# Performance work log

Hardware: AMD Instinct MI355X
Metric: run time of the kernel (lower is better)

## Reference

```python
import jax, jax.numpy as jnp
import numpy as np
from jax import lax

BN_EPS = 1e-5


def setup_inputs() -> dict:
    key = jax.random.key(0)
    ks = jax.random.split(key, 3)
    B, N, D = 96, 20, 2048
    return {
        "x": jax.random.normal(ks[0], (B, N, D), dtype=jnp.float32),
        "conv_w": jax.random.normal(ks[1], (D, 2 * D), dtype=jnp.float32) * 0.02,
        "conv_b": jax.random.normal(ks[2], (D,), dtype=jnp.float32) * 0.02,
        "bn_gamma": jnp.ones((D,), dtype=jnp.float32),
        "bn_beta": jnp.zeros((D,), dtype=jnp.float32),
        "bn_mean": jnp.zeros((D,), dtype=jnp.float32),
        "bn_var": jnp.ones((D,), dtype=jnp.float32),
        "n_neighbor": 10,
    }


def reference(x, conv_w, conv_b, bn_gamma, bn_beta, bn_mean, bn_var, n_neighbor):
    # x: [B, N, D] -> xt: [B, D, N] (channels-first point cloud of view features)
    xt = jnp.transpose(x, (0, 2, 1))
    B, D, N = xt.shape
    k = int(n_neighbor)

    # pairwise squared distances: [B, N, N]
    sq = jnp.sum(xt * xt, axis=1, keepdims=True)            # [B, 1, N]
    inner = jnp.einsum("bdn,bdm->bnm", xt, xt)              # [B, N, N]
    adj = sq + (-2.0) * inner + jnp.transpose(sq, (0, 2, 1))

    # k nearest neighbors (smallest distance) -> idx [B, N, k]
    _, nn_idx = lax.top_k(-adj, k)

    # gather neighbor features without the O(N^2) expand: [B, D, N, k]
    neighbors = jax.vmap(lambda xb, idx: xb[:, idx])(xt, nn_idx)

    center = xt[:, :, :, None]                              # [B, D, N, 1]
    edge = jnp.concatenate(
        [jnp.broadcast_to(center, (B, D, N, k)), neighbors - center], axis=1
    )                                                       # [B, 2D, N, k]

    # 1x1 conv (GEMM over channel dim) + BatchNorm (inference) + ReLU
    y = jnp.einsum("oc,bcnk->bonk", conv_w, edge) + conv_b[None, :, None, None]
    inv = bn_gamma / jnp.sqrt(bn_var + BN_EPS)
    y = y * inv[None, :, None, None] + (bn_beta - bn_mean * inv)[None, :, None, None]
    y = jax.nn.relu(y)

    # max over neighbors, then max over points -> [B, D, 1, 1]
    y = jnp.max(y, axis=-1, keepdims=True)
    y = jnp.max(y, axis=2, keepdims=True)
    return y
```

## Files before the change

### kernel.cpp

```cpp
#include <hip/hip_runtime.h>
#include <hip/hip_bf16.h>
#include <math.h>

#define BN_EPS 1e-5f
#define B_  96
#define N_  20
#define D_  2048
#define K_  10
#define M_  (B_*N_)
#define R_  (2*D_)

typedef __attribute__((ext_vector_type(8))) short bf16x8;
typedef __attribute__((ext_vector_type(4))) float f32x4;
typedef __attribute__((ext_vector_type(8))) unsigned short ushort8;

static __device__ __forceinline__ unsigned short f2bf(float f) {
  unsigned int u = __builtin_bit_cast(unsigned int, f);
  u = u + 0x7fffu + ((u >> 16) & 1u);
  return (unsigned short)(u >> 16);
}

#define GLOAD_LDS16(g, l) \
  __builtin_amdgcn_global_load_lds((const __attribute__((address_space(1))) void*)(g), \
                                   (__attribute__((address_space(3))) void*)(l), 16, 0, 0)

__global__ __launch_bounds__(512, 2) void prep_kernel(const float* __restrict__ x,
                                                      const float* __restrict__ cw,
                                                      int* __restrict__ nn_idx,
                                                      unsigned short* __restrict__ Xb,
                                                      unsigned short* __restrict__ Wn)
{
  int t = threadIdx.x;
  if (blockIdx.x >= B_) {
    int cb = blockIdx.x - B_;
    for (int i = cb*512 + t; i < R_*D_/8; i += 416*512) {
      int r = i >> 8;
      int k = (i & 255) * 8;
      const float* src = cw + (size_t)(r >> 1) * R_ + ((r & 1) << 11) + k;
      float4 a = *(const float4*)src, c = *(const float4*)(src + 4);
      ushort8 o = { f2bf(a.x), f2bf(a.y), f2bf(a.z), f2bf(a.w),
                    f2bf(c.x), f2bf(c.y), f2bf(c.z), f2bf(c.w) };
      *((ushort8*)Wn + i) = o;
    }
    return;
  }
  int b = blockIdx.x, w = t >> 6, lane = t & 63;
  __shared__ float innr[N_*N_];
  __shared__ float adjl[N_*N_];
  const float* xb = x + (size_t)b * N_ * D_;
  int n1 = w, n2 = w + 8, n3 = (w < 4) ? 16 + w : -1;
  float4 c1[8], c2[8], c3[8];
  const float4* p1 = (const float4*)(xb + n1 * D_);
  const float4* p2 = (const float4*)(xb + n2 * D_);
  #pragma unroll
  for (int j = 0; j < 8; ++j) { c1[j] = p1[lane + 64*j]; c2[j] = p2[lane + 64*j]; }
  if (n3 >= 0) {
    const float4* p3 = (const float4*)(xb + n3 * D_);
    #pragma unroll
    for (int j = 0; j < 8; ++j) c3[j] = p3[lane + 64*j];
  }
  for (int m = n1; m < N_; ++m) {
    bool d2 = (m >= n2), d3 = (n3 >= 0) && (m >= n3);
    const float4* pm = (const float4*)(xb + m * D_);
    float s1 = 0.f, s2 = 0.f, s3 = 0.f;
    #pragma unroll
    for (int j = 0; j < 8; ++j) {
      float4 v = pm[lane + 64*j];
      s1 = fmaf(c1[j].x, v.x, fmaf(c1[j].y, v.y, fmaf(c1[j].z, v.z, fmaf(c1[j].w, v.w, s1))));
      if (d2) s2 = fmaf(c2[j].x, v.x, fmaf(c2[j].y, v.y, fmaf(c2[j].z, v.z, fmaf(c2[j].w, v.w, s2))));
      if (d3) s3 = fmaf(c3[j].x, v.x, fmaf(c3[j].y, v.y, fmaf(c3[j].z, v.z, fmaf(c3[j].w, v.w, s3))));
    }
    #pragma unroll
    for (int off = 32; off > 0; off >>= 1) {
      s1 += __shfl_xor(s1, off, 64);
      if (d2) s2 += __shfl_xor(s2, off, 64);
      if (d3) s3 += __shfl_xor(s3, off, 64);
    }
    if (lane == 0) {
      innr[n1*N_+m] = s1; innr[m*N_+n1] = s1;
      if (d2) { innr[n2*N_+m] = s2; innr[m*N_+n2] = s2; }
      if (d3) { innr[n3*N_+m] = s3; innr[m*N_+n3] = s3; }
    }
  }
  __syncthreads();
  for (int p = t; p < N_*N_; p += 512) {
    int n = p / N_, m = p % N_;
    adjl[p] = innr[n*N_+n] + innr[m*N_+m] - 2.f * innr[p];
  }
  __syncthreads();
  if (t < N_) {
    int n = t;
    unsigned mask = 0;
    for (int it = 0; it < K_; ++it) {
      float bv = INFINITY; int bi = 0;
      for (int m = 0; m < N_; ++m) {
        if (!((mask >> m) & 1u)) {
          float v = adjl[n*N_+m];
          if (v < bv) { bv = v; bi = m; }
        }
      }
      mask |= 1u << bi;
      nn_idx[(b*N_ + n)*K_ + it] = bi;
    }
  }
  unsigned short* xo = Xb + (size_t)b * N_ * D_;
  for (int i = t; i < N_*D_/8; i += 512) {
    const float4* src = (const float4*)xb + (size_t)i * 2;
    float4 a = src[0], c = src[1];
    ushort8 o = { f2bf(a.x), f2bf(a.y), f2bf(a.z), f2bf(a.w),
                  f2bf(c.x), f2bf(c.y), f2bf(c.z), f2bf(c.w) };
    *((ushort8*)xo + i) = o;
  }
}

__global__ __launch_bounds__(256, 3) void fused_gemm(
    const unsigned short* __restrict__ Xb, const unsigned short* __restrict__ Wn,
    const int* __restrict__ nn_idx, const float* __restrict__ conv_b,
    const float* __restrict__ gamma, const float* __restrict__ beta,
    const float* __restrict__ mean, const float* __restrict__ var,
    float* __restrict__ out)
{
  __shared__ __align__(16) char smem[53248];
  float* Cl  = (float*)smem;
  int*   idxl = (int*)(smem + 40960);

  int flat = blockIdx.y * 24 + blockIdx.x;
  int nf = (flat & 7) * 96 + (flat >> 3);
  int bx = nf % 24, by = nf / 24;

  int t = threadIdx.x, lane = t & 63, w = t >> 6;
  int m0 = bx * 80, b0 = bx * 4;
  int r0 = by * 128, o0 = by * 64;
  int rowsel = lane & 15, ksel = lane >> 4;

  f32x4 acc[5][2] = {};

  auto stage = [&](int sel, int k0) {
    unsigned short* Asb = (unsigned short*)(smem + sel*26624);
    unsigned short* Bsb = (unsigned short*)(smem + sel*26624 + 10240);
    #pragma unroll
    for (int i = 0; i < 3; ++i) {
      int fl = i*256 + t;
      if (fl < 640) {
        int row = fl >> 3, kc = fl & 7;
        GLOAD_LDS16(Xb + (size_t)(m0 + row) * D_ + k0 + ((kc ^ (row & 7)) << 3),
                    Asb + fl*8);
      }
    }
    #pragma unroll
    for (int i = 0; i < 4; ++i) {
      int fl = i*256 + t;
      int row = fl >> 3, kc = fl & 7;
      GLOAD_LDS16(Wn + (size_t)(r0 + row) * D_ + k0 + ((kc ^ (row & 7)) << 3),
                  Bsb + fl*8);
    }
  };

  auto compute = [&](int sel) {
    unsigned short* Asb = (unsigned short*)(smem + sel*26624);
    unsigned short* Bsb = (unsigned short*)(smem + sel*26624 + 10240);
    #pragma unroll
    for (int ks = 0; ks < 2; ++ks) {
      int swz = ((ks*4 + ksel) ^ (rowsel & 7)) << 3;
      bf16x8 a[5], bfr[2];
      #pragma unroll
      for (int mi = 0; mi < 5; ++mi)
        a[mi] = *(const bf16x8*)(Asb + (mi*16 + rowsel)*64 + swz);
      #pragma unroll
      for (int ri = 0; ri < 2; ++ri)
        bfr[ri] = *(const bf16x8*)(Bsb + (w*32 + ri*16 + rowsel)*64 + swz);
      #pragma unroll
      for (int mi = 0; mi < 5; ++mi)
        #pragma unroll
        for (int ri = 0; ri < 2; ++ri)
          acc[mi][ri] = __builtin_amdgcn_mfma_f32_16x16x32_bf16(a[mi], bfr[ri], acc[mi][ri], 0, 0, 0);
    }
  };

  stage(0, 0);
  #pragma unroll 1
  for (int kt = 0; kt < D_/64; ++kt) {
    __builtin_amdgcn_s_barrier();
    __builtin_amdgcn_sched_barrier(0);
    if (kt + 1 < D_/64) {
      stage((kt+1) & 1, (kt+1)*64);
      if (w < 2) { asm volatile("s_waitcnt vmcnt(7)" ::: "memory"); }
      else       { asm volatile("s_waitcnt vmcnt(6)" ::: "memory"); }
    } else {
      asm volatile("s_waitcnt vmcnt(0)" ::: "memory");
    }
    __builtin_amdgcn_sched_barrier(0);
    __builtin_amdgcn_s_barrier();
    __builtin_amdgcn_sched_barrier(0);
    compute(kt & 1);
  }
  __syncthreads();

  #pragma unroll
  for (int mi = 0; mi < 5; ++mi)
    #pragma unroll
    for (int ri = 0; ri < 2; ++ri)
      #pragma unroll
      for (int rg = 0; rg < 4; ++rg)
        Cl[(mi*16 + ksel*4 + rg)*128 + w*32 + ri*16 + rowsel] = acc[mi][ri][rg];
  for (int i = t; i < 4*N_*K_; i += 256) idxl[i] = nn_idx[b0*N_*K_ + i];
  __syncthreads();

  int bb = w, oo = lane;
  int og = o0 + oo;
  float invv  = gamma[og] / sqrtf(var[og] + BN_EPS);
  float shift = fmaf(-mean[og], invv, beta[og]);
  float bias  = conv_b[og];
  float best = 0.f;
  int rbase = bb * N_;
  for (int n = 0; n < N_; ++n) {
    float Pv = Cl[(rbase + n)*128 + oo*2];
    float Qn = Cl[(rbase + n)*128 + oo*2 + 1];
    float aa = Pv - Qn + bias;
    const int* ix = idxl + bb*N_*K_ + n*K_;
    #pragma unroll
    for (int kk = 0; kk < K_; ++kk) {
      int j = ix[kk];
      float v = fmaf(aa + Cl[(rbase + j)*128 + oo*2 + 1], invv, shift);
      best = fmaxf(best, v);
    }
  }
  out[(size_t)(b0 + bb) * D_ + og] = best;
}

extern "C" void kernel_launch(void* const* d_in, const int* in_sizes, int n_in,
                              void* d_out, int out_size, void* d_ws, size_t ws_size,
                              hipStream_t stream)
{
  const float* x      = (const float*)d_in[0];
  const float* conv_w = (const float*)d_in[1];
  const float* conv_b = (const float*)d_in[2];
  const float* gamma  = (const float*)d_in[3];
  const float* beta   = (const float*)d_in[4];
  const float* mean   = (const float*)d_in[5];
  const float* var    = (const float*)d_in[6];

  int* nn_idx = (int*)d_ws;
  unsigned short* Xb = (unsigned short*)((char*)d_ws + 76800);
  unsigned short* Wn = (unsigned short*)((char*)d_ws + 76800 + (size_t)M_*D_*2);

  prep_kernel<<<512, 512, 0, stream>>>(x, conv_w, nn_idx, Xb, Wn);
  fused_gemm<<<dim3(24, 32), 256, 0, stream>>>(
      Xb, Wn, nn_idx, conv_b, gamma, beta, mean, var, (float*)d_out);
}
```

Measured before the change: 78.59 us.

## Load GEMM weight fragments directly into registers and widen weight conversion grid

```diff
diff --git a/kernel.cpp b/kernel.cpp
--- a/kernel.cpp
+++ b/kernel.cpp
@@ -32,16 +32,31 @@
 {
   int t = threadIdx.x;
   if (blockIdx.x >= B_) {
-    int cb = blockIdx.x - B_;
-    for (int i = cb*512 + t; i < R_*D_/8; i += 416*512) {
-      int r = i >> 8;
-      int k = (i & 255) * 8;
-      const float* src = cw + (size_t)(r >> 1) * R_ + ((r & 1) << 11) + k;
-      float4 a = *(const float4*)src, c = *(const float4*)(src + 4);
-      ushort8 o = { f2bf(a.x), f2bf(a.y), f2bf(a.z), f2bf(a.w),
-                    f2bf(c.x), f2bf(c.y), f2bf(c.z), f2bf(c.w) };
-      *((ushort8*)Wn + i) = o;
-    }
+    int i0 = (blockIdx.x - B_) * 512 + t;
+    auto srcp = [&](int i) {
+      int r = i >> 8, k = (i & 255) * 8;
+      return cw + (size_t)(r >> 1) * R_ + ((r & 1) << 11) + k;
+    };
+    const float* s0 = srcp(i0);
+    const float* s1 = srcp(i0 + 262144);
+    const float* s2 = srcp(i0 + 524288);
+    const float* s3 = srcp(i0 + 786432);
+    float4 a0 = *(const float4*)s0, c0 = *(const float4*)(s0 + 4);
+    float4 a1 = *(const float4*)s1, c1 = *(const float4*)(s1 + 4);
+    float4 a2 = *(const float4*)s2, c2 = *(const float4*)(s2 + 4);
+    float4 a3 = *(const float4*)s3, c3 = *(const float4*)(s3 + 4);
+    ushort8 o0 = { f2bf(a0.x), f2bf(a0.y), f2bf(a0.z), f2bf(a0.w),
+                   f2bf(c0.x), f2bf(c0.y), f2bf(c0.z), f2bf(c0.w) };
+    ushort8 o1 = { f2bf(a1.x), f2bf(a1.y), f2bf(a1.z), f2bf(a1.w),
+                   f2bf(c1.x), f2bf(c1.y), f2bf(c1.z), f2bf(c1.w) };
+    ushort8 o2 = { f2bf(a2.x), f2bf(a2.y), f2bf(a2.z), f2bf(a2.w),
+                   f2bf(c2.x), f2bf(c2.y), f2bf(c2.z), f2bf(c2.w) };
+    ushort8 o3 = { f2bf(a3.x), f2bf(a3.y), f2bf(a3.z), f2bf(a3.w),
+                   f2bf(c3.x), f2bf(c3.y), f2bf(c3.z), f2bf(c3.w) };
+    *((ushort8*)Wn + i0)          = o0;
+    *((ushort8*)Wn + i0 + 262144) = o1;
+    *((ushort8*)Wn + i0 + 524288) = o2;
+    *((ushort8*)Wn + i0 + 786432) = o3;
     return;
   }
   int b = blockIdx.x, w = t >> 6, lane = t & 63;
@@ -120,7 +135,7 @@
     const float* __restrict__ mean, const float* __restrict__ var,
     float* __restrict__ out)
 {
-  __shared__ __align__(16) char smem[53248];
+  __shared__ __align__(16) char smem[44160];
   float* Cl  = (float*)smem;
   int*   idxl = (int*)(smem + 40960);
 
@@ -135,9 +150,10 @@
 
   f32x4 acc[5][2] = {};
 
-  auto stage = [&](int sel, int k0) {
-    unsigned short* Asb = (unsigned short*)(smem + sel*26624);
-    unsigned short* Bsb = (unsigned short*)(smem + sel*26624 + 10240);
+  const unsigned short* wnBase = Wn + (size_t)(r0 + w*32 + rowsel) * D_ + ksel*8;
+
+  auto stageA = [&](int sel, int k0) {
+    unsigned short* Asb = (unsigned short*)(smem + sel*10240);
     #pragma unroll
     for (int i = 0; i < 3; ++i) {
       int fl = i*256 + t;
@@ -147,54 +163,46 @@
                     Asb + fl*8);
       }
     }
-    #pragma unroll
-    for (int i = 0; i < 4; ++i) {
-      int fl = i*256 + t;
-      int row = fl >> 3, kc = fl & 7;
-      GLOAD_LDS16(Wn + (size_t)(r0 + row) * D_ + k0 + ((kc ^ (row & 7)) << 3),
-                  Bsb + fl*8);
-    }
   };
 
-  auto compute = [&](int sel) {
-    unsigned short* Asb = (unsigned short*)(smem + sel*26624);
-    unsigned short* Bsb = (unsigned short*)(smem + sel*26624 + 10240);
+  auto loadB = [&](bf16x8 (&bb)[2][2], int kt) {
+    #pragma unroll
+    for (int ri = 0; ri < 2; ++ri)
+      #pragma unroll
+      for (int ks = 0; ks < 2; ++ks)
+        bb[ri][ks] = *(const bf16x8*)(wnBase + (size_t)(ri*16) * D_ + kt*64 + ks*32);
+  };
+
+  auto computeStep = [&](int sel, const bf16x8 (&bb)[2][2]) {
+    unsigned short* Asb = (unsigned short*)(smem + sel*10240);
     #pragma unroll
     for (int ks = 0; ks < 2; ++ks) {
       int swz = ((ks*4 + ksel) ^ (rowsel & 7)) << 3;
-      bf16x8 a[5], bfr[2];
+      bf16x8 a[5];
       #pragma unroll
       for (int mi = 0; mi < 5; ++mi)
         a[mi] = *(const bf16x8*)(Asb + (mi*16 + rowsel)*64 + swz);
-      #pragma unroll
-      for (int ri = 0; ri < 2; ++ri)
-        bfr[ri] = *(const bf16x8*)(Bsb + (w*32 + ri*16 + rowsel)*64 + swz);
       #pragma unroll
       for (int mi = 0; mi < 5; ++mi)
         #pragma unroll
         for (int ri = 0; ri < 2; ++ri)
-          acc[mi][ri] = __builtin_amdgcn_mfma_f32_16x16x32_bf16(a[mi], bfr[ri], acc[mi][ri], 0, 0, 0);
+          acc[mi][ri] = __builtin_amdgcn_mfma_f32_16x16x32_bf16(a[mi], bb[ri][ks], acc[mi][ri], 0, 0, 0);
     }
   };
 
-  stage(0, 0);
+  bf16x8 bEven[2][2], bOdd[2][2];
+  stageA(0, 0);
+  loadB(bEven, 0);
+  __syncthreads();
   #pragma unroll 1
-  for (int kt = 0; kt < D_/64; ++kt) {
-    __builtin_amdgcn_s_barrier();
-    __builtin_amdgcn_sched_barrier(0);
-    if (kt + 1 < D_/64) {
-      stage((kt+1) & 1, (kt+1)*64);
-      if (w < 2) { asm volatile("s_waitcnt vmcnt(7)" ::: "memory"); }
-      else       { asm volatile("s_waitcnt vmcnt(6)" ::: "memory"); }
-    } else {
-      asm volatile("s_waitcnt vmcnt(0)" ::: "memory");
-    }
-    __builtin_amdgcn_sched_barrier(0);
-    __builtin_amdgcn_s_barrier();
-    __builtin_amdgcn_sched_barrier(0);
-    compute(kt & 1);
-  }
-  __syncthreads();
+  for (int kt = 0; kt < D_/64; kt += 2) {
+    if (kt + 1 < D_/64) { stageA(1, (kt+1)*64); loadB(bOdd, kt+1); }
+    computeStep(0, bEven);
+    __syncthreads();
+    if (kt + 2 < D_/64) { stageA(0, (kt+2)*64); loadB(bEven, kt+2); }
+    computeStep(1, bOdd);
+    __syncthreads();
+  }
 
   #pragma unroll
   for (int mi = 0; mi < 5; ++mi)
@@ -244,7 +252,7 @@
   unsigned short* Xb = (unsigned short*)((char*)d_ws + 76800);
   unsigned short* Wn = (unsigned short*)((char*)d_ws + 76800 + (size_t)M_*D_*2);
 
-  prep_kernel<<<512, 512, 0, stream>>>(x, conv_w, nn_idx, Xb, Wn);
+  prep_kernel<<<B_ + 512, 512, 0, stream>>>(x, conv_w, nn_idx, Xb, Wn);
   fused_gemm<<<dim3(24, 32), 256, 0, stream>>>(
       Xb, Wn, nn_idx, conv_b, gamma, beta, mean, var, (float*)d_out);
 }
```

Measured after the change: 97.19 us. 23.7% more time.

## Fuse weight bf16 conversion into GEMM B-tile staging via registers

Applied to the files above, without the earlier changes.

```diff
diff --git a/kernel.cpp b/kernel.cpp
--- a/kernel.cpp
+++ b/kernel.cpp
@@ -25,25 +25,10 @@
                                    (__attribute__((address_space(3))) void*)(l), 16, 0, 0)
 
 __global__ __launch_bounds__(512, 2) void prep_kernel(const float* __restrict__ x,
-                                                      const float* __restrict__ cw,
                                                       int* __restrict__ nn_idx,
-                                                      unsigned short* __restrict__ Xb,
-                                                      unsigned short* __restrict__ Wn)
+                                                      unsigned short* __restrict__ Xb)
 {
   int t = threadIdx.x;
-  if (blockIdx.x >= B_) {
-    int cb = blockIdx.x - B_;
-    for (int i = cb*512 + t; i < R_*D_/8; i += 416*512) {
-      int r = i >> 8;
-      int k = (i & 255) * 8;
-      const float* src = cw + (size_t)(r >> 1) * R_ + ((r & 1) << 11) + k;
-      float4 a = *(const float4*)src, c = *(const float4*)(src + 4);
-      ushort8 o = { f2bf(a.x), f2bf(a.y), f2bf(a.z), f2bf(a.w),
-                    f2bf(c.x), f2bf(c.y), f2bf(c.z), f2bf(c.w) };
-      *((ushort8*)Wn + i) = o;
-    }
-    return;
-  }
   int b = blockIdx.x, w = t >> 6, lane = t & 63;
   __shared__ float innr[N_*N_];
   __shared__ float adjl[N_*N_];
@@ -114,7 +99,7 @@
 }
 
 __global__ __launch_bounds__(256, 3) void fused_gemm(
-    const unsigned short* __restrict__ Xb, const unsigned short* __restrict__ Wn,
+    const unsigned short* __restrict__ Xb, const float* __restrict__ cw,
     const int* __restrict__ nn_idx, const float* __restrict__ conv_b,
     const float* __restrict__ gamma, const float* __restrict__ beta,
     const float* __restrict__ mean, const float* __restrict__ var,
@@ -135,9 +120,8 @@
 
   f32x4 acc[5][2] = {};
 
-  auto stage = [&](int sel, int k0) {
+  auto stageA = [&](int sel, int k0) {
     unsigned short* Asb = (unsigned short*)(smem + sel*26624);
-    unsigned short* Bsb = (unsigned short*)(smem + sel*26624 + 10240);
     #pragma unroll
     for (int i = 0; i < 3; ++i) {
       int fl = i*256 + t;
@@ -147,12 +131,30 @@
                     Asb + fl*8);
       }
     }
+  };
+
+  auto loadB = [&](float4 (&bf)[8], int k0) {
     #pragma unroll
     for (int i = 0; i < 4; ++i) {
       int fl = i*256 + t;
-      int row = fl >> 3, kc = fl & 7;
-      GLOAD_LDS16(Wn + (size_t)(r0 + row) * D_ + k0 + ((kc ^ (row & 7)) << 3),
-                  Bsb + fl*8);
+      int row = fl >> 3, kcg = (fl & 7) ^ (row & 7);
+      int r = r0 + row;
+      const float* src = cw + (size_t)(r >> 1) * R_ + ((r & 1) << 11) + k0 + kcg*8;
+      bf[2*i]   = *(const float4*)src;
+      bf[2*i+1] = *(const float4*)(src + 4);
+    }
+  };
+
+  auto writeB = [&](const float4 (&bf)[8], int sel) {
+    unsigned short* Bsb = (unsigned short*)(smem + sel*26624 + 10240);
+    #pragma unroll
+    for (int i = 0; i < 4; ++i) {
+      int fl = i*256 + t;
+      const float4& a = bf[2*i];
+      const float4& c = bf[2*i+1];
+      ushort8 o = { f2bf(a.x), f2bf(a.y), f2bf(a.z), f2bf(a.w),
+                    f2bf(c.x), f2bf(c.y), f2bf(c.z), f2bf(c.w) };
+      *(ushort8*)(Bsb + fl*8) = o;
     }
   };
 
@@ -177,24 +179,21 @@
     }
   };
 
-  stage(0, 0);
+  float4 bf[8];
+  loadB(bf, 0);
+  stageA(0, 0);
+  writeB(bf, 0);
+  __syncthreads();
   #pragma unroll 1
   for (int kt = 0; kt < D_/64; ++kt) {
-    __builtin_amdgcn_s_barrier();
-    __builtin_amdgcn_sched_barrier(0);
     if (kt + 1 < D_/64) {
-      stage((kt+1) & 1, (kt+1)*64);
-      if (w < 2) { asm volatile("s_waitcnt vmcnt(7)" ::: "memory"); }
-      else       { asm volatile("s_waitcnt vmcnt(6)" ::: "memory"); }
-    } else {
-      asm volatile("s_waitcnt vmcnt(0)" ::: "memory");
-    }
-    __builtin_amdgcn_sched_barrier(0);
-    __builtin_amdgcn_s_barrier();
-    __builtin_amdgcn_sched_barrier(0);
+      loadB(bf, (kt+1)*64);
+      stageA((kt+1) & 1, (kt+1)*64);
+    }
     compute(kt & 1);
-  }
-  __syncthreads();
+    if (kt + 1 < D_/64) writeB(bf, (kt+1) & 1);
+    __syncthreads();
+  }
 
   #pragma unroll
   for (int mi = 0; mi < 5; ++mi)
@@ -242,9 +241,8 @@
 
   int* nn_idx = (int*)d_ws;
   unsigned short* Xb = (unsigned short*)((char*)d_ws + 76800);
-  unsigned short* Wn = (unsigned short*)((char*)d_ws + 76800 + (size_t)M_*D_*2);
-
-  prep_kernel<<<512, 512, 0, stream>>>(x, conv_w, nn_idx, Xb, Wn);
+
+  prep_kernel<<<B_, 512, 0, stream>>>(x, nn_idx, Xb);
   fused_gemm<<<dim3(24, 32), 256, 0, stream>>>(
-      Xb, Wn, nn_idx, conv_b, gamma, beta, mean, var, (float*)d_out);
-}
+      Xb, conv_w, nn_idx, conv_b, gamma, beta, mean, var, (float*)d_out);
+}
```

New measurement: 92.62 us. +17.9%, slower.
